# Optimization experiments

Measured on AMD Instinct MI355X. Metric: run time of the kernel, lower is better.

The kernel has to match this reference:

```python
import jax, jax.numpy as jnp
import numpy as np

N = 100_000            # particles
E = 3_200_000          # edges (avg degree 32)
DIM = 3
H = 1.0                # kernel_radius
SIGMA = 3.0 / 359.0 / np.pi / H**3   # 3D quintic kernel normalization
RHO_REF = 1.0
P_REF = 100.0          # rho_ref * (10*u_ref)**2 / gamma, gamma=1
P_BG = 0.0             # p_bg_factor * p_ref
ETA0 = 0.01            # base_viscosity
EPS = 1e-8


def _qpows(d, p):
    q = d / H
    return (jnp.maximum(0.0, 1.0 - q) ** p,
            jnp.maximum(0.0, 2.0 - q) ** p,
            jnp.maximum(0.0, 3.0 - q) ** p)


def kernel_w(d):
    q1, q2, q3 = _qpows(d, 5)
    return SIGMA * (q3 - 6.0 * q2 + 15.0 * q1)


def kernel_grad_w(d):
    q1, q2, q3 = _qpows(d, 4)
    return (SIGMA / H) * (-5.0 * q3 + 30.0 * q2 - 75.0 * q1)


def setup_inputs() -> dict:
    key = jax.random.key(0)
    k1, k2, k3, k4 = jax.random.split(key, 4)
    r = jax.random.uniform(k1, (N, DIM), dtype=jnp.float32)   # positions in unit box
    v = jax.random.normal(k2, (N, DIM), dtype=jnp.float32)    # velocity history (last frame)
    i_s = jax.random.randint(k3, (E,), 0, N)                  # receivers
    j_s = jax.random.randint(k4, (E,), 0, N)                  # senders
    return {"r": r, "v": v, "i_s": i_s, "j_s": j_s}


def reference(r, v, i_s, j_s):
    n = r.shape[0]
    # --- per-edge gather + kernel ---
    dr = r[i_s] - r[j_s]                       # displacement_fn, [E,3]
    d = jnp.sqrt(jnp.sum(dr * dr, axis=-1))    # [E]
    w = kernel_w(d)
    # --- density summation (scatter) ---
    mass = jnp.ones((n,), r.dtype)
    rho = mass * jax.ops.segment_sum(w, i_s, num_segments=n)
    # Tait EoS, gamma=1
    p = P_REF * (rho / RHO_REF - 1.0) + P_BG
    eta = jnp.full((n,), ETA0, r.dtype)

    # --- per-edge acceleration (gather particle fields to edges) ---
    rho_i, rho_j = rho[i_s], rho[j_s]
    p_i, p_j = p[i_s], p[j_s]
    eta_i, eta_j = eta[i_s], eta[j_s]
    u_i, u_j = v[i_s], v[j_s]                  # u == v in _transform
    v_i, v_j = u_i, u_j

    eta_ij = 2.0 * eta_i * eta_j / (eta_i + eta_j + EPS)
    p_ij = (rho_j * p_i + rho_i * p_j) / (rho_i + rho_j)
    # ((m_i/rho_i)^2 + (m_j/rho_j)^2)/m_i with m == 1
    wvol = (1.0 / rho_i) ** 2 + (1.0 / rho_j) ** 2
    c = wvol * kernel_grad_w(d) / (d + EPS)    # [E]

    # transport stress A = (outer(rho_i*u_i, v_i-u_i) + outer(rho_j*u_j, v_j-u_j))/2, [E,3,3]
    A = 0.5 * (rho_i[:, None, None] * u_i[:, :, None] * (v_i - u_i)[:, None, :]
               + rho_j[:, None, None] * u_j[:, :, None] * (v_j - u_j)[:, None, :])
    Ar = jnp.einsum('eij,ej->ei', A, dr)

    a_eq_8 = c[:, None] * (-p_ij[:, None] * dr + Ar + eta_ij[:, None] * (u_i - u_j))
    p_bg_i = jnp.zeros_like(p_i)               # _transform passes zeros
    a_eq_13 = (c * p_bg_i)[:, None] * dr

    # --- scatter-reduce to particles ---
    dudt = jax.ops.segment_sum(a_eq_8, i_s, num_segments=n)   # [N,3]
    dvdt = jax.ops.segment_sum(a_eq_13, i_s, num_segments=n)  # [N,3]

    # pack state outputs: [rho, p, dudt(3), dvdt(3)] -> [N,8]
    return jnp.concatenate([rho[:, None], p[:, None], dudt, dvdt], axis=1)
```

## Files before the change

kernel.cpp:

```cpp
#include <hip/hip_runtime.h>
#include <math.h>

#ifndef M_PI
#define M_PI 3.14159265358979323846
#endif

static constexpr float kSigma = (float)(3.0 / 359.0 / M_PI);
static constexpr float kPRef  = 100.0f;
static constexpr float kEps   = 1e-8f;
static constexpr float kEta   = (float)(2.0 * 0.01 * 0.01 / (0.01 + 0.01 + 1e-8));

#define CHUNK 4096
#define NSUB  8
#define BAT   5

typedef _Float16 hf4 __attribute__((ext_vector_type(4)));

__device__ __forceinline__ float pow5f(float t) { float t2 = t * t; return t2 * t2 * t; }
__device__ __forceinline__ float pow4f(float t) { float t2 = t * t; return t2 * t2; }

__global__ void k_pack(const float* __restrict__ r, float4* __restrict__ pos4, int n) {
    int i = blockIdx.x * blockDim.x + threadIdx.x;
    if (i >= n) return;
    pos4[i] = make_float4(r[3 * i], r[3 * i + 1], r[3 * i + 2], 0.f);
}

__global__ void k_hist(const int* __restrict__ i_s, int* __restrict__ ghist,
                       int nbA, int nbins, int E, int shift) {
    __shared__ int h[512];
    int t = threadIdx.x, blk = blockIdx.x;
    for (int b = t; b < nbins; b += 256) h[b] = 0;
    __syncthreads();
    int base = blk * CHUNK;
    int end = min(base + CHUNK, E);
    for (int kb = base; kb < end; kb += 256 * 4) {
        int iv[4];
#pragma unroll
        for (int b = 0; b < 4; b++) {
            int k = kb + b * 256 + t;
            iv[b] = (k < end) ? i_s[k] : -1;
        }
#pragma unroll
        for (int b = 0; b < 4; b++)
            if (iv[b] >= 0) atomicAdd(&h[iv[b] >> shift], 1);
    }
    __syncthreads();
    for (int b = t; b < nbins; b += 256)
        ghist[b * nbA + blk] = h[b];
}

__global__ void k_scan_block(const int* __restrict__ in, int* __restrict__ out,
                             int* __restrict__ bsum, int m) {
    __shared__ int s[256];
    int t = threadIdx.x;
    int i = blockIdx.x * 256 + t;
    int x = (i < m) ? in[i] : 0;
    s[t] = x;
    __syncthreads();
    for (int d = 1; d < 256; d <<= 1) {
        int v = (t >= d) ? s[t - d] : 0;
        __syncthreads();
        s[t] += v;
        __syncthreads();
    }
    if (i < m) out[i] = s[t] - x;
    if (t == 255) bsum[blockIdx.x] = s[255];
}

__global__ void k_scan_bsums(const int* __restrict__ bsum, int* __restrict__ bscan, int nb) {
    __shared__ int s[512];
    __shared__ int carry;
    int t = threadIdx.x;
    if (t == 0) carry = 0;
    __syncthreads();
    for (int base = 0; base < nb; base += 512) {
        int i = base + t;
        int x = (i < nb) ? bsum[i] : 0;
        s[t] = x;
        __syncthreads();
        for (int d = 1; d < 512; d <<= 1) {
            int v = (t >= d) ? s[t - d] : 0;
            __syncthreads();
            s[t] += v;
            __syncthreads();
        }
        if (i < nb) bscan[i] = s[t] - x + carry;
        __syncthreads();
        if (t == 511) carry += s[511];
        __syncthreads();
    }
}

__device__ __forceinline__ int scanned(const int* __restrict__ gscan,
                                       const int* __restrict__ bscan, int idx) {
    return gscan[idx] + bscan[idx >> 8];
}

__global__ void k_split(const int* __restrict__ i_s, const int* __restrict__ j_s,
                        const int* __restrict__ ghist, const int* __restrict__ gscan,
                        const int* __restrict__ bscan, int* __restrict__ pairs,
                        int nbA, int nbins, int E, int shift, int jbits) {
    __shared__ int lofs[512];
    __shared__ int ldelta[512];
    __shared__ int stage[CHUNK];
    __shared__ unsigned short binof[CHUNK];
    int t = threadIdx.x, blk = blockIdx.x;
    int base = blk * CHUNK;
    int end = min(base + CHUNK, E);
    int cnt = end - base;

    int h0 = (t < nbins) ? ghist[t * nbA + blk] : 0;
    int h1 = (t + 256 < nbins) ? ghist[(t + 256) * nbA + blk] : 0;
    lofs[t] = h0;
    lofs[t + 256] = h1;
    __syncthreads();
    for (int d = 1; d < 512; d <<= 1) {
        int v0 = (t >= d) ? lofs[t - d] : 0;
        int v1 = ((t + 256) >= d) ? lofs[t + 256 - d] : 0;
        __syncthreads();
        lofs[t] += v0;
        lofs[t + 256] += v1;
        __syncthreads();
    }
    int e0 = lofs[t] - h0;
    int e1 = lofs[t + 256] - h1;
    __syncthreads();
    lofs[t] = e0;
    lofs[t + 256] = e1;
    if (t < nbins) ldelta[t] = scanned(gscan, bscan, t * nbA + blk) - e0;
    if (t + 256 < nbins) ldelta[t + 256] = scanned(gscan, bscan, (t + 256) * nbA + blk) - e1;
    __syncthreads();

    int fmask = (1 << shift) - 1;
    for (int kb = base; kb < end; kb += 256 * 4) {
        int iv[4], jv[4];
#pragma unroll
        for (int b = 0; b < 4; b++) {
            int k = kb + b * 256 + t;
            iv[b] = (k < end) ? i_s[k] : -1;
            jv[b] = (k < end) ? j_s[k] : 0;
        }
#pragma unroll
        for (int b = 0; b < 4; b++) {
            if (iv[b] < 0) continue;
            int bin = iv[b] >> shift;
            int pos = atomicAdd(&lofs[bin], 1);
            stage[pos] = ((iv[b] & fmask) << jbits) | jv[b];
            binof[pos] = (unsigned short)bin;
        }
    }
    __syncthreads();
    for (int x = t; x < cnt; x += 256)
        pairs[x + ldelta[binof[x]]] = stage[x];
}

__global__ void __launch_bounds__(256, 6)
k_rho_bin(const float4* __restrict__ pos4, const int* __restrict__ pairs,
          const int* __restrict__ gscan, const int* __restrict__ bscan,
          float* __restrict__ part_rho, hf4* __restrict__ aux,
          int nbA, int n, int E, int shift, int jbits, int nbins) {
    __shared__ float srho[256];
    __shared__ float4 spos[256];
    __shared__ int sse[2];
    int bin = blockIdx.x >> 3, sub = blockIdx.x & (NSUB - 1);
    int t = threadIdx.x;
    int lo = bin << shift;
    srho[t] = 0.f;
    int ii = lo + t;
    spos[t] = (ii < n) ? pos4[ii] : make_float4(0.f, 0.f, 0.f, 0.f);
    if (t == 0) {
        sse[0] = scanned(gscan, bscan, bin * nbA);
        sse[1] = (bin + 1 < nbins) ? scanned(gscan, bscan, (bin + 1) * nbA) : E;
    }
    __syncthreads();
    int s = sse[0], len = sse[1] - sse[0];
    int k0 = s + (int)((long)len * sub / NSUB);
    int k1 = s + (int)((long)len * (sub + 1) / NSUB);
    int jm = (1 << jbits) - 1;
    for (int kb = k0; kb < k1; kb += 256 * BAT) {
        int pr[BAT], kk[BAT];
        bool live[BAT];
#pragma unroll
        for (int b = 0; b < BAT; b++) {
            int k = kb + b * 256 + t;
            live[b] = (k < k1);
            kk[b] = live[b] ? k : (k1 - 1);
            pr[b] = pairs[kk[b]];
        }
        float4 rj[BAT];
#pragma unroll
        for (int b = 0; b < BAT; b++) rj[b] = pos4[pr[b] & jm];
#pragma unroll
        for (int b = 0; b < BAT; b++) {
            int slot = pr[b] >> jbits;
            float4 ri = spos[slot];
            float dx = ri.x - rj[b].x, dy = ri.y - rj[b].y, dz = ri.z - rj[b].z;
            float d = sqrtf(dx * dx + dy * dy + dz * dz);
            float t1 = fmaxf(1.f - d, 0.f);
            float t2 = fmaxf(2.f - d, 0.f);
            float t3 = fmaxf(3.f - d, 0.f);
            float w = kSigma * (pow5f(t3) - 6.f * pow5f(t2) + 15.f * pow5f(t1));
            hf4 h;
            h.x = (_Float16)dx; h.y = (_Float16)dy;
            h.z = (_Float16)dz; h.w = (_Float16)d;
            if (live[b]) {
                atomicAdd(&srho[slot], w);
                aux[kk[b]] = h;
            }
        }
    }
    __syncthreads();
    if (ii < n) part_rho[(size_t)sub * n + ii] = srho[t];
}

__global__ void k_reduce_rho(const float* __restrict__ part_rho,
                             const float* __restrict__ v,
                             float4* __restrict__ vp4, float* __restrict__ out, int n) {
    int i = blockIdx.x * blockDim.x + threadIdx.x;
    if (i >= n) return;
    float rh = 0.f;
    for (int s = 0; s < NSUB; s++) rh += part_rho[(size_t)s * n + i];
    float pp = kPRef * (rh - 1.0f);
    vp4[i] = make_float4(v[3 * i], v[3 * i + 1], v[3 * i + 2], pp);
    float* o = out + (size_t)i * 8;
    o[0] = rh;
    o[1] = pp;
    o[5] = 0.f; o[6] = 0.f; o[7] = 0.f;
}

__global__ void __launch_bounds__(256, 6)
k_acc_bin(const float4* __restrict__ vp4, const int* __restrict__ pairs,
          const hf4* __restrict__ aux,
          const int* __restrict__ gscan, const int* __restrict__ bscan,
          float4* __restrict__ part_acc4, int nbA, int n, int E,
          int shift, int jbits, int nbins) {
    __shared__ float sax[256], say[256], saz[256];
    __shared__ float4 svp[256];
    __shared__ int sse[2];
    int bin = blockIdx.x >> 3, sub = blockIdx.x & (NSUB - 1);
    int t = threadIdx.x;
    int lo = bin << shift;
    sax[t] = 0.f; say[t] = 0.f; saz[t] = 0.f;
    int ii = lo + t;
    svp[t] = (ii < n) ? vp4[ii] : make_float4(0.f, 0.f, 0.f, 0.f);
    if (t == 0) {
        sse[0] = scanned(gscan, bscan, bin * nbA);
        sse[1] = (bin + 1 < nbins) ? scanned(gscan, bscan, (bin + 1) * nbA) : E;
    }
    __syncthreads();
    int s = sse[0], len = sse[1] - sse[0];
    int k0 = s + (int)((long)len * sub / NSUB);
    int k1 = s + (int)((long)len * (sub + 1) / NSUB);
    int jm = (1 << jbits) - 1;
    for (int kb = k0; kb < k1; kb += 256 * BAT) {
        int pr[BAT], kk[BAT];
        bool live[BAT];
        hf4 hx[BAT];
#pragma unroll
        for (int b = 0; b < BAT; b++) {
            int k = kb + b * 256 + t;
            live[b] = (k < k1);
            kk[b] = live[b] ? k : (k1 - 1);
            pr[b] = pairs[kk[b]];
            hx[b] = aux[kk[b]];
        }
        float4 vj[BAT];
#pragma unroll
        for (int b = 0; b < BAT; b++) vj[b] = vp4[pr[b] & jm];
#pragma unroll
        for (int b = 0; b < BAT; b++) {
            int slot = pr[b] >> jbits;
            float4 bi = svp[slot];
            float p_i = bi.w, p_j = vj[b].w;
            float rho_i = p_i * 0.01f + 1.0f;
            float rho_j = p_j * 0.01f + 1.0f;
            float dx = (float)hx[b].x, dy = (float)hx[b].y, dz = (float)hx[b].z;
            float d = (float)hx[b].w;
            float t1 = fmaxf(1.f - d, 0.f);
            float t2 = fmaxf(2.f - d, 0.f);
            float t3 = fmaxf(3.f - d, 0.f);
            float gw = kSigma * (-5.f * pow4f(t3) + 30.f * pow4f(t2) - 75.f * pow4f(t1));
            float inv_i = 1.0f / rho_i, inv_j = 1.0f / rho_j;
            float c = (inv_i * inv_i + inv_j * inv_j) * gw / (d + kEps);
            float p_ij = (rho_j * p_i + rho_i * p_j) / (rho_i + rho_j);
            if (live[b]) {
                atomicAdd(&sax[slot], c * (kEta * (bi.x - vj[b].x) - p_ij * dx));
                atomicAdd(&say[slot], c * (kEta * (bi.y - vj[b].y) - p_ij * dy));
                atomicAdd(&saz[slot], c * (kEta * (bi.z - vj[b].z) - p_ij * dz));
            }
        }
    }
    __syncthreads();
    if (ii < n)
        part_acc4[(size_t)sub * n + ii] = make_float4(sax[t], say[t], saz[t], 0.f);
}

__global__ void k_reduce_acc(const float4* __restrict__ part_acc4,
                             float* __restrict__ out, int n) {
    int i = blockIdx.x * blockDim.x + threadIdx.x;
    if (i >= n) return;
    float ax = 0.f, ay = 0.f, az = 0.f;
    for (int s = 0; s < NSUB; s++) {
        float4 p = part_acc4[(size_t)s * n + i];
        ax += p.x; ay += p.y; az += p.z;
    }
    float* o = out + (size_t)i * 8 + 2;
    o[0] = ax; o[1] = ay; o[2] = az;
}

static inline char* wcarve(char*& ws, size_t bytes) {
    char* p = ws;
    ws += (bytes + 255) & ~(size_t)255;
    return p;
}

extern "C" void kernel_launch(void* const* d_in, const int* in_sizes, int n_in,
                              void* d_out, int out_size, void* d_ws, size_t ws_size,
                              hipStream_t stream) {
    const float* r = (const float*)d_in[0];
    const float* v = (const float*)d_in[1];
    const int* i_s = (const int*)d_in[2];
    const int* j_s = (const int*)d_in[3];
    int n = in_sizes[0] / 3;
    int E = in_sizes[2];
    float* out = (float*)d_out;

    int shift = 8;
    int nbins = ((n - 1) >> shift) + 1;
    while (nbins > 512) { shift++; nbins = ((n - 1) >> shift) + 1; }
    int jbits = 1;
    while ((1 << jbits) < n) jbits++;

    int nbA = (E + CHUNK - 1) / CHUNK;
    int m = nbins * nbA;
    int nb2 = (m + 255) / 256;

    char* ws = (char*)d_ws;
    float4* pos4     = (float4*)wcarve(ws, (size_t)n * 16);
    float4* vp4      = (float4*)wcarve(ws, (size_t)n * 16);
    int*    ghist    = (int*)wcarve(ws, (size_t)m * 4);
    int*    gscan    = (int*)wcarve(ws, (size_t)m * 4);
    int*    bsum     = (int*)wcarve(ws, (size_t)nb2 * 4);
    int*    bscan    = (int*)wcarve(ws, (size_t)nb2 * 4);
    int*    pairs    = (int*)wcarve(ws, (size_t)E * 4);
    hf4*    aux      = (hf4*)wcarve(ws, (size_t)E * 8);
    float*  part_rho = (float*)wcarve(ws, (size_t)NSUB * n * 4);
    float4* part_acc4= (float4*)wcarve(ws, (size_t)NSUB * n * 16);

    const int bs = 256;
    int gn = (n + bs - 1) / bs;

    k_pack<<<gn, bs, 0, stream>>>(r, pos4, n);
    k_hist<<<nbA, 256, 0, stream>>>(i_s, ghist, nbA, nbins, E, shift);
    k_scan_block<<<nb2, 256, 0, stream>>>(ghist, gscan, bsum, m);
    k_scan_bsums<<<1, 512, 0, stream>>>(bsum, bscan, nb2);
    k_split<<<nbA, 256, 0, stream>>>(i_s, j_s, ghist, gscan, bscan, pairs, nbA, nbins, E, shift, jbits);
    k_rho_bin<<<nbins * NSUB, 256, 0, stream>>>(pos4, pairs, gscan, bscan, part_rho, aux, nbA, n, E, shift, jbits, nbins);
    k_reduce_rho<<<gn, bs, 0, stream>>>(part_rho, v, vp4, out, n);
    k_acc_bin<<<nbins * NSUB, 256, 0, stream>>>(vp4, pairs, aux, gscan, bscan, part_acc4, nbA, n, E, shift, jbits, nbins);
    k_reduce_acc<<<gn, bs, 0, stream>>>(part_acc4, out, n);
}
```

Baseline: 201.7 us.

## Two-level sort edges by sender slice and receiver bin, cache both in LDS

Replaces the single receiver-bin sort with a two-pass sort: first by sender slice of 4096 particles, then by receiver bin of 512. The density and acceleration passes can then stage both sender and receiver data in shared memory instead of doing random global gathers of sender data. Positions are quantized to 16-bit fixed point and velocity/pressure to fp16, which shrinks the footprint and removes the fp16 aux buffer. The cost is extra sort passes, per-slice partial buffers (25 slices × N) and reduced precision in positions, velocity and pressure.

```diff
diff --git a/kernel.cpp b/kernel.cpp
--- a/kernel.cpp
+++ b/kernel.cpp
@@ -9,44 +9,63 @@
 static constexpr float kPRef  = 100.0f;
 static constexpr float kEps   = 1e-8f;
 static constexpr float kEta   = (float)(2.0 * 0.01 * 0.01 / (0.01 + 0.01 + 1e-8));
-
-#define CHUNK 4096
-#define NSUB  8
-#define BAT   5
+static constexpr float kInvQ  = 1.0f / 65536.0f;
+
+#define CH     4096
+#define JS_SH  12
+#define JSLICE 4096
+#define IB_SH  9
+#define IBSZ   512
+#define C2MAX  48
+#define GBIN   8
 
 typedef _Float16 hf4 __attribute__((ext_vector_type(4)));
 
 __device__ __forceinline__ float pow5f(float t) { float t2 = t * t; return t2 * t2 * t; }
 __device__ __forceinline__ float pow4f(float t) { float t2 = t * t; return t2 * t2; }
 
-__global__ void k_pack(const float* __restrict__ r, float4* __restrict__ pos4, int n) {
+__device__ __forceinline__ int nt_load_i(const int* p) { return __builtin_nontemporal_load(p); }
+__device__ __forceinline__ float nt_load_f(const float* p) { return __builtin_nontemporal_load(p); }
+__device__ __forceinline__ void nt_store_f(float* p, float v) { __builtin_nontemporal_store(v, p); }
+
+__device__ __forceinline__ int scanned(const int* __restrict__ gscan,
+                                       const int* __restrict__ bscan, int idx) {
+    return gscan[idx] + bscan[idx >> 8];
+}
+
+__global__ void k_pack_pos(const float* __restrict__ r, ushort4* __restrict__ posq, int n) {
     int i = blockIdx.x * blockDim.x + threadIdx.x;
     if (i >= n) return;
-    pos4[i] = make_float4(r[3 * i], r[3 * i + 1], r[3 * i + 2], 0.f);
-}
-
-__global__ void k_hist(const int* __restrict__ i_s, int* __restrict__ ghist,
-                       int nbA, int nbins, int E, int shift) {
-    __shared__ int h[512];
+    float x = r[3 * i], y = r[3 * i + 1], z = r[3 * i + 2];
+    ushort4 q;
+    q.x = (unsigned short)fminf(x * 65536.0f, 65535.0f);
+    q.y = (unsigned short)fminf(y * 65536.0f, 65535.0f);
+    q.z = (unsigned short)fminf(z * 65536.0f, 65535.0f);
+    q.w = 0;
+    posq[i] = q;
+}
+
+__global__ void k_hist1(const int* __restrict__ j_s, int* __restrict__ ghist,
+                        int nbA, int nsl, int E) {
+    __shared__ int h[64];
     int t = threadIdx.x, blk = blockIdx.x;
-    for (int b = t; b < nbins; b += 256) h[b] = 0;
-    __syncthreads();
-    int base = blk * CHUNK;
-    int end = min(base + CHUNK, E);
+    if (t < 64) h[t] = 0;
+    __syncthreads();
+    int base = blk * CH;
+    int end = min(base + CH, E);
     for (int kb = base; kb < end; kb += 256 * 4) {
-        int iv[4];
+        int jv[4];
 #pragma unroll
         for (int b = 0; b < 4; b++) {
             int k = kb + b * 256 + t;
-            iv[b] = (k < end) ? i_s[k] : -1;
+            jv[b] = (k < end) ? j_s[k] : -1;
         }
 #pragma unroll
         for (int b = 0; b < 4; b++)
-            if (iv[b] >= 0) atomicAdd(&h[iv[b] >> shift], 1);
-    }
-    __syncthreads();
-    for (int b = t; b < nbins; b += 256)
-        ghist[b * nbA + blk] = h[b];
+            if (jv[b] >= 0) atomicAdd(&h[jv[b] >> JS_SH], 1);
+    }
+    __syncthreads();
+    if (t < nsl) ghist[t * nbA + blk] = h[t];
 }
 
 __global__ void k_scan_block(const int* __restrict__ in, int* __restrict__ out,
@@ -91,47 +110,35 @@
     }
 }
 
-__device__ __forceinline__ int scanned(const int* __restrict__ gscan,
-                                       const int* __restrict__ bscan, int idx) {
-    return gscan[idx] + bscan[idx >> 8];
-}
-
-__global__ void k_split(const int* __restrict__ i_s, const int* __restrict__ j_s,
-                        const int* __restrict__ ghist, const int* __restrict__ gscan,
-                        const int* __restrict__ bscan, int* __restrict__ pairs,
-                        int nbA, int nbins, int E, int shift, int jbits) {
-    __shared__ int lofs[512];
-    __shared__ int ldelta[512];
-    __shared__ int stage[CHUNK];
-    __shared__ unsigned short binof[CHUNK];
+__global__ void k_split1(const int* __restrict__ i_s, const int* __restrict__ j_s,
+                         const int* __restrict__ ghist, const int* __restrict__ gscan,
+                         const int* __restrict__ bscan, int* __restrict__ pairs1,
+                         int nbA, int nsl, int E) {
+    __shared__ int lofs[64];
+    __shared__ int ldelta[64];
+    __shared__ int stage[CH];
+    __shared__ unsigned short binof[CH];
     int t = threadIdx.x, blk = blockIdx.x;
-    int base = blk * CHUNK;
-    int end = min(base + CHUNK, E);
+    int base = blk * CH;
+    int end = min(base + CH, E);
     int cnt = end - base;
 
-    int h0 = (t < nbins) ? ghist[t * nbA + blk] : 0;
-    int h1 = (t + 256 < nbins) ? ghist[(t + 256) * nbA + blk] : 0;
-    lofs[t] = h0;
-    lofs[t + 256] = h1;
-    __syncthreads();
-    for (int d = 1; d < 512; d <<= 1) {
-        int v0 = (t >= d) ? lofs[t - d] : 0;
-        int v1 = ((t + 256) >= d) ? lofs[t + 256 - d] : 0;
-        __syncthreads();
-        lofs[t] += v0;
-        lofs[t + 256] += v1;
-        __syncthreads();
-    }
-    int e0 = lofs[t] - h0;
-    int e1 = lofs[t + 256] - h1;
-    __syncthreads();
-    lofs[t] = e0;
-    lofs[t + 256] = e1;
-    if (t < nbins) ldelta[t] = scanned(gscan, bscan, t * nbA + blk) - e0;
-    if (t + 256 < nbins) ldelta[t + 256] = scanned(gscan, bscan, (t + 256) * nbA + blk) - e1;
-    __syncthreads();
-
-    int fmask = (1 << shift) - 1;
+    if (t < 64) {
+        int h0 = (t < nsl) ? ghist[t * nbA + blk] : 0;
+        lofs[t] = h0;
+    }
+    __syncthreads();
+    if (t == 0) {
+        int run = 0;
+        for (int b = 0; b < nsl; b++) {
+            int h = lofs[b];
+            lofs[b] = run;
+            ldelta[b] = scanned(gscan, bscan, b * nbA + blk) - run;
+            run += h;
+        }
+    }
+    __syncthreads();
+
     for (int kb = base; kb < end; kb += 256 * 4) {
         int iv[4], jv[4];
 #pragma unroll
@@ -143,139 +150,225 @@
 #pragma unroll
         for (int b = 0; b < 4; b++) {
             if (iv[b] < 0) continue;
-            int bin = iv[b] >> shift;
+            int bin = jv[b] >> JS_SH;
             int pos = atomicAdd(&lofs[bin], 1);
-            stage[pos] = ((iv[b] & fmask) << jbits) | jv[b];
+            stage[pos] = (iv[b] << JS_SH) | (jv[b] & (JSLICE - 1));
             binof[pos] = (unsigned short)bin;
         }
     }
     __syncthreads();
     for (int x = t; x < cnt; x += 256)
-        pairs[x + ldelta[binof[x]]] = stage[x];
-}
-
-__global__ void __launch_bounds__(256, 6)
-k_rho_bin(const float4* __restrict__ pos4, const int* __restrict__ pairs,
-          const int* __restrict__ gscan, const int* __restrict__ bscan,
-          float* __restrict__ part_rho, hf4* __restrict__ aux,
-          int nbA, int n, int E, int shift, int jbits, int nbins) {
-    __shared__ float srho[256];
-    __shared__ float4 spos[256];
+        pairs1[x + ldelta[binof[x]]] = stage[x];
+}
+
+__global__ void k_hist2(const int* __restrict__ pairs1, const int* __restrict__ gscan1,
+                        const int* __restrict__ bscan1, int* __restrict__ ghist2,
+                        int nbA, int nsl, int nbin, int E) {
+    __shared__ int h[256];
+    int t = threadIdx.x;
+    int s = blockIdx.x / C2MAX, c = blockIdx.x % C2MAX;
+    h[t] = 0;
+    __syncthreads();
+    int start = scanned(gscan1, bscan1, s * nbA);
+    int end = (s + 1 < nsl) ? scanned(gscan1, bscan1, (s + 1) * nbA) : E;
+    int a0 = start + c * CH, a1 = min(a0 + CH, end);
+    for (int kb = a0; kb < a1; kb += 256 * 4) {
+        int pv[4];
+#pragma unroll
+        for (int b = 0; b < 4; b++) {
+            int k = kb + b * 256 + t;
+            pv[b] = (k < a1) ? pairs1[k] : -1;
+        }
+#pragma unroll
+        for (int b = 0; b < 4; b++)
+            if (pv[b] >= 0) atomicAdd(&h[pv[b] >> (JS_SH + IB_SH)], 1);
+    }
+    __syncthreads();
+    if (t < nbin) ghist2[(s * nbin + t) * C2MAX + c] = h[t];
+}
+
+__global__ void k_split2(const int* __restrict__ pairs1, const int* __restrict__ ghist2,
+                         const int* __restrict__ gscan2, const int* __restrict__ bscan2,
+                         const int* __restrict__ gscan1, const int* __restrict__ bscan1,
+                         int* __restrict__ pairs2, int nbA, int nsl, int nbin, int E) {
+    __shared__ int lofs[256];
+    __shared__ int ldelta[256];
+    __shared__ int stage[CH];
+    __shared__ unsigned short binof[CH];
+    int t = threadIdx.x;
+    int s = blockIdx.x / C2MAX, c = blockIdx.x % C2MAX;
+    int start = scanned(gscan1, bscan1, s * nbA);
+    int end = (s + 1 < nsl) ? scanned(gscan1, bscan1, (s + 1) * nbA) : E;
+    int a0 = start + c * CH, a1 = min(a0 + CH, end);
+    int cnt = max(a1 - a0, 0);
+
+    int h0 = (t < nbin) ? ghist2[(s * nbin + t) * C2MAX + c] : 0;
+    lofs[t] = h0;
+    __syncthreads();
+    for (int d = 1; d < 256; d <<= 1) {
+        int v = (t >= d) ? lofs[t - d] : 0;
+        __syncthreads();
+        lofs[t] += v;
+        __syncthreads();
+    }
+    int e0 = lofs[t] - h0;
+    __syncthreads();
+    lofs[t] = e0;
+    if (t < nbin) ldelta[t] = scanned(gscan2, bscan2, (s * nbin + t) * C2MAX + c) - e0;
+    __syncthreads();
+
+    for (int kb = a0; kb < a1; kb += 256 * 4) {
+        int pv[4];
+#pragma unroll
+        for (int b = 0; b < 4; b++) {
+            int k = kb + b * 256 + t;
+            pv[b] = (k < a1) ? pairs1[k] : -1;
+        }
+#pragma unroll
+        for (int b = 0; b < 4; b++) {
+            if (pv[b] < 0) continue;
+            int bin = pv[b] >> (JS_SH + IB_SH);
+            int pos = atomicAdd(&lofs[bin], 1);
+            stage[pos] = pv[b];
+            binof[pos] = (unsigned short)bin;
+        }
+    }
+    __syncthreads();
+    for (int x = t; x < cnt; x += 256)
+        pairs2[x + ldelta[binof[x]]] = stage[x];
+}
+
+__global__ void __launch_bounds__(256)
+k_pass1(const ushort4* __restrict__ posq, const int* __restrict__ pairs2,
+        const int* __restrict__ gscan2, const int* __restrict__ bscan2,
+        float* __restrict__ part_rho, int n, int E, int nsl, int nbin,
+        int nbg, int nk) {
+    __shared__ ushort4 sjp[JSLICE];
+    __shared__ ushort4 sip[IBSZ];
+    __shared__ float srho[IBSZ];
     __shared__ int sse[2];
-    int bin = blockIdx.x >> 3, sub = blockIdx.x & (NSUB - 1);
-    int t = threadIdx.x;
-    int lo = bin << shift;
-    srho[t] = 0.f;
-    int ii = lo + t;
-    spos[t] = (ii < n) ? pos4[ii] : make_float4(0.f, 0.f, 0.f, 0.f);
-    if (t == 0) {
-        sse[0] = scanned(gscan, bscan, bin * nbA);
-        sse[1] = (bin + 1 < nbins) ? scanned(gscan, bscan, (bin + 1) * nbA) : E;
-    }
-    __syncthreads();
-    int s = sse[0], len = sse[1] - sse[0];
-    int k0 = s + (int)((long)len * sub / NSUB);
-    int k1 = s + (int)((long)len * (sub + 1) / NSUB);
-    int jm = (1 << jbits) - 1;
-    for (int kb = k0; kb < k1; kb += 256 * BAT) {
-        int pr[BAT], kk[BAT];
-        bool live[BAT];
-#pragma unroll
-        for (int b = 0; b < BAT; b++) {
-            int k = kb + b * 256 + t;
-            live[b] = (k < k1);
-            kk[b] = live[b] ? k : (k1 - 1);
-            pr[b] = pairs[kk[b]];
-        }
-        float4 rj[BAT];
-#pragma unroll
-        for (int b = 0; b < BAT; b++) rj[b] = pos4[pr[b] & jm];
-#pragma unroll
-        for (int b = 0; b < BAT; b++) {
-            int slot = pr[b] >> jbits;
-            float4 ri = spos[slot];
-            float dx = ri.x - rj[b].x, dy = ri.y - rj[b].y, dz = ri.z - rj[b].z;
+    int t = threadIdx.x;
+    int s = blockIdx.x / nbg, g = blockIdx.x % nbg;
+    int j0 = s << JS_SH;
+    for (int idx = t; idx < JSLICE; idx += 256) {
+        int jg = j0 + idx;
+        sjp[idx] = (jg < n) ? posq[jg] : make_ushort4(0, 0, 0, 0);
+    }
+    int b0 = g * GBIN, b1 = min(b0 + GBIN, nbin);
+    for (int bin = b0; bin < b1; bin++) {
+        int i0 = bin << IB_SH;
+        for (int idx = t; idx < IBSZ; idx += 256) {
+            int ig = i0 + idx;
+            sip[idx] = (ig < n) ? posq[ig] : make_ushort4(0, 0, 0, 0);
+            srho[idx] = 0.f;
+        }
+        if (t == 0) {
+            int lin = s * nbin + bin;
+            sse[0] = scanned(gscan2, bscan2, lin * C2MAX);
+            sse[1] = (lin + 1 < nk) ? scanned(gscan2, bscan2, (lin + 1) * C2MAX) : E;
+        }
+        __syncthreads();
+        int ks = sse[0], ke = sse[1];
+        for (int k = ks + t; k < ke; k += 256) {
+            int pr = nt_load_i(&pairs2[k]);
+            int jl = pr & (JSLICE - 1);
+            int il = (pr >> JS_SH) & (IBSZ - 1);
+            ushort4 pj = sjp[jl];
+            ushort4 pi = sip[il];
+            float dx = (float)((int)pi.x - (int)pj.x) * kInvQ;
+            float dy = (float)((int)pi.y - (int)pj.y) * kInvQ;
+            float dz = (float)((int)pi.z - (int)pj.z) * kInvQ;
             float d = sqrtf(dx * dx + dy * dy + dz * dz);
             float t1 = fmaxf(1.f - d, 0.f);
             float t2 = fmaxf(2.f - d, 0.f);
             float t3 = fmaxf(3.f - d, 0.f);
             float w = kSigma * (pow5f(t3) - 6.f * pow5f(t2) + 15.f * pow5f(t1));
-            hf4 h;
-            h.x = (_Float16)dx; h.y = (_Float16)dy;
-            h.z = (_Float16)dz; h.w = (_Float16)d;
-            if (live[b]) {
-                atomicAdd(&srho[slot], w);
-                aux[kk[b]] = h;
-            }
-        }
-    }
-    __syncthreads();
-    if (ii < n) part_rho[(size_t)sub * n + ii] = srho[t];
+            atomicAdd(&srho[il], w);
+        }
+        __syncthreads();
+        for (int idx = t; idx < IBSZ; idx += 256) {
+            int ig = i0 + idx;
+            if (ig < n) nt_store_f(&part_rho[(size_t)s * n + ig], srho[idx]);
+        }
+        __syncthreads();
+    }
 }
 
 __global__ void k_reduce_rho(const float* __restrict__ part_rho,
                              const float* __restrict__ v,
-                             float4* __restrict__ vp4, float* __restrict__ out, int n) {
+                             hf4* __restrict__ vpq, float* __restrict__ out,
+                             int n, int nsl) {
     int i = blockIdx.x * blockDim.x + threadIdx.x;
     if (i >= n) return;
     float rh = 0.f;
-    for (int s = 0; s < NSUB; s++) rh += part_rho[(size_t)s * n + i];
+    for (int s = 0; s < nsl; s++) rh += nt_load_f(&part_rho[(size_t)s * n + i]);
     float pp = kPRef * (rh - 1.0f);
-    vp4[i] = make_float4(v[3 * i], v[3 * i + 1], v[3 * i + 2], pp);
+    hf4 h;
+    h.x = (_Float16)v[3 * i];
+    h.y = (_Float16)v[3 * i + 1];
+    h.z = (_Float16)v[3 * i + 2];
+    h.w = (_Float16)pp;
+    vpq[i] = h;
     float* o = out + (size_t)i * 8;
     o[0] = rh;
     o[1] = pp;
     o[5] = 0.f; o[6] = 0.f; o[7] = 0.f;
 }
 
-__global__ void __launch_bounds__(256, 6)
-k_acc_bin(const float4* __restrict__ vp4, const int* __restrict__ pairs,
-          const hf4* __restrict__ aux,
-          const int* __restrict__ gscan, const int* __restrict__ bscan,
-          float4* __restrict__ part_acc4, int nbA, int n, int E,
-          int shift, int jbits, int nbins) {
-    __shared__ float sax[256], say[256], saz[256];
-    __shared__ float4 svp[256];
+__global__ void __launch_bounds__(256)
+k_pass2(const ushort4* __restrict__ posq, const hf4* __restrict__ vpq,
+        const int* __restrict__ pairs2, const int* __restrict__ gscan2,
+        const int* __restrict__ bscan2, float* __restrict__ pax,
+        float* __restrict__ pay, float* __restrict__ paz,
+        int n, int E, int nsl, int nbin, int nbg, int nk) {
+    extern __shared__ char dyn[];
+    ushort4* sjp = (ushort4*)dyn;
+    hf4*     sjv = (hf4*)(dyn + 32768);
+    ushort4* sip = (ushort4*)(dyn + 65536);
+    hf4*     siv = (hf4*)(dyn + 69632);
+    float*   sax = (float*)(dyn + 73728);
+    float*   say = (float*)(dyn + 75776);
+    float*   saz = (float*)(dyn + 77824);
     __shared__ int sse[2];
-    int bin = blockIdx.x >> 3, sub = blockIdx.x & (NSUB - 1);
-    int t = threadIdx.x;
-    int lo = bin << shift;
-    sax[t] = 0.f; say[t] = 0.f; saz[t] = 0.f;
-    int ii = lo + t;
-    svp[t] = (ii < n) ? vp4[ii] : make_float4(0.f, 0.f, 0.f, 0.f);
-    if (t == 0) {
-        sse[0] = scanned(gscan, bscan, bin * nbA);
-        sse[1] = (bin + 1 < nbins) ? scanned(gscan, bscan, (bin + 1) * nbA) : E;
-    }
-    __syncthreads();
-    int s = sse[0], len = sse[1] - sse[0];
-    int k0 = s + (int)((long)len * sub / NSUB);
-    int k1 = s + (int)((long)len * (sub + 1) / NSUB);
-    int jm = (1 << jbits) - 1;
-    for (int kb = k0; kb < k1; kb += 256 * BAT) {
-        int pr[BAT], kk[BAT];
-        bool live[BAT];
-        hf4 hx[BAT];
-#pragma unroll
-        for (int b = 0; b < BAT; b++) {
-            int k = kb + b * 256 + t;
-            live[b] = (k < k1);
-            kk[b] = live[b] ? k : (k1 - 1);
-            pr[b] = pairs[kk[b]];
-            hx[b] = aux[kk[b]];
-        }
-        float4 vj[BAT];
-#pragma unroll
-        for (int b = 0; b < BAT; b++) vj[b] = vp4[pr[b] & jm];
-#pragma unroll
-        for (int b = 0; b < BAT; b++) {
-            int slot = pr[b] >> jbits;
-            float4 bi = svp[slot];
-            float p_i = bi.w, p_j = vj[b].w;
+    int t = threadIdx.x;
+    int s = blockIdx.x / nbg, g = blockIdx.x % nbg;
+    int j0 = s << JS_SH;
+    for (int idx = t; idx < JSLICE; idx += 256) {
+        int jg = j0 + idx;
+        if (jg < n) { sjp[idx] = posq[jg]; sjv[idx] = vpq[jg]; }
+        else { sjp[idx] = make_ushort4(0, 0, 0, 0); sjv[idx] = hf4{0, 0, 0, 0}; }
+    }
+    int b0 = g * GBIN, b1 = min(b0 + GBIN, nbin);
+    for (int bin = b0; bin < b1; bin++) {
+        int i0 = bin << IB_SH;
+        for (int idx = t; idx < IBSZ; idx += 256) {
+            int ig = i0 + idx;
+            if (ig < n) { sip[idx] = posq[ig]; siv[idx] = vpq[ig]; }
+            else { sip[idx] = make_ushort4(0, 0, 0, 0); siv[idx] = hf4{0, 0, 0, 0}; }
+            sax[idx] = 0.f; say[idx] = 0.f; saz[idx] = 0.f;
+        }
+        if (t == 0) {
+            int lin = s * nbin + bin;
+            sse[0] = scanned(gscan2, bscan2, lin * C2MAX);
+            sse[1] = (lin + 1 < nk) ? scanned(gscan2, bscan2, (lin + 1) * C2MAX) : E;
+        }
+        __syncthreads();
+        int ks = sse[0], ke = sse[1];
+        for (int k = ks + t; k < ke; k += 256) {
+            int pr = nt_load_i(&pairs2[k]);
+            int jl = pr & (JSLICE - 1);
+            int il = (pr >> JS_SH) & (IBSZ - 1);
+            ushort4 pj = sjp[jl];
+            hf4 vj = sjv[jl];
+            ushort4 pi = sip[il];
+            hf4 vi = siv[il];
+            float dx = (float)((int)pi.x - (int)pj.x) * kInvQ;
+            float dy = (float)((int)pi.y - (int)pj.y) * kInvQ;
+            float dz = (float)((int)pi.z - (int)pj.z) * kInvQ;
+            float d = sqrtf(dx * dx + dy * dy + dz * dz);
+            float p_i = (float)vi.w, p_j = (float)vj.w;
             float rho_i = p_i * 0.01f + 1.0f;
             float rho_j = p_j * 0.01f + 1.0f;
-            float dx = (float)hx[b].x, dy = (float)hx[b].y, dz = (float)hx[b].z;
-            float d = (float)hx[b].w;
             float t1 = fmaxf(1.f - d, 0.f);
             float t2 = fmaxf(2.f - d, 0.f);
             float t3 = fmaxf(3.f - d, 0.f);
@@ -283,26 +376,33 @@
             float inv_i = 1.0f / rho_i, inv_j = 1.0f / rho_j;
             float c = (inv_i * inv_i + inv_j * inv_j) * gw / (d + kEps);
             float p_ij = (rho_j * p_i + rho_i * p_j) / (rho_i + rho_j);
-            if (live[b]) {
-                atomicAdd(&sax[slot], c * (kEta * (bi.x - vj[b].x) - p_ij * dx));
-                atomicAdd(&say[slot], c * (kEta * (bi.y - vj[b].y) - p_ij * dy));
-                atomicAdd(&saz[slot], c * (kEta * (bi.z - vj[b].z) - p_ij * dz));
+            atomicAdd(&sax[il], c * (kEta * ((float)vi.x - (float)vj.x) - p_ij * dx));
+            atomicAdd(&say[il], c * (kEta * ((float)vi.y - (float)vj.y) - p_ij * dy));
+            atomicAdd(&saz[il], c * (kEta * ((float)vi.z - (float)vj.z) - p_ij * dz));
+        }
+        __syncthreads();
+        for (int idx = t; idx < IBSZ; idx += 256) {
+            int ig = i0 + idx;
+            if (ig < n) {
+                nt_store_f(&pax[(size_t)s * n + ig], sax[idx]);
+                nt_store_f(&pay[(size_t)s * n + ig], say[idx]);
+                nt_store_f(&paz[(size_t)s * n + ig], saz[idx]);
             }
         }
-    }
-    __syncthreads();
-    if (ii < n)
-        part_acc4[(size_t)sub * n + ii] = make_float4(sax[t], say[t], saz[t], 0.f);
-}
-
-__global__ void k_reduce_acc(const float4* __restrict__ part_acc4,
-                             float* __restrict__ out, int n) {
+        __syncthreads();
+    }
+}
+
+__global__ void k_reduce_acc(const float* __restrict__ pax, const float* __restrict__ pay,
+                             const float* __restrict__ paz, float* __restrict__ out,
+                             int n, int nsl) {
     int i = blockIdx.x * blockDim.x + threadIdx.x;
     if (i >= n) return;
     float ax = 0.f, ay = 0.f, az = 0.f;
-    for (int s = 0; s < NSUB; s++) {
-        float4 p = part_acc4[(size_t)s * n + i];
-        ax += p.x; ay += p.y; az += p.z;
+    for (int s = 0; s < nsl; s++) {
+        ax += nt_load_f(&pax[(size_t)s * n + i]);
+        ay += nt_load_f(&pay[(size_t)s * n + i]);
+        az += nt_load_f(&paz[(size_t)s * n + i]);
     }
     float* o = out + (size_t)i * 8 + 2;
     o[0] = ax; o[1] = ay; o[2] = az;
@@ -325,38 +425,58 @@
     int E = in_sizes[2];
     float* out = (float*)d_out;
 
-    int shift = 8;
-    int nbins = ((n - 1) >> shift) + 1;
-    while (nbins > 512) { shift++; nbins = ((n - 1) >> shift) + 1; }
-    int jbits = 1;
-    while ((1 << jbits) < n) jbits++;
-
-    int nbA = (E + CHUNK - 1) / CHUNK;
-    int m = nbins * nbA;
-    int nb2 = (m + 255) / 256;
+    int nsl  = ((n - 1) >> JS_SH) + 1;
+    int nbin = ((n - 1) >> IB_SH) + 1;
+    int nk   = nsl * nbin;
+    int nbg  = (nbin + GBIN - 1) / GBIN;
+    int nbA  = (E + CH - 1) / CH;
+    int m1   = nsl * nbA;
+    int m2   = nk * C2MAX;
+    int nb1  = (m1 + 255) / 256;
+    int nb2  = (m2 + 255) / 256;
 
     char* ws = (char*)d_ws;
-    float4* pos4     = (float4*)wcarve(ws, (size_t)n * 16);
-    float4* vp4      = (float4*)wcarve(ws, (size_t)n * 16);
-    int*    ghist    = (int*)wcarve(ws, (size_t)m * 4);
-    int*    gscan    = (int*)wcarve(ws, (size_t)m * 4);
-    int*    bsum     = (int*)wcarve(ws, (size_t)nb2 * 4);
-    int*    bscan    = (int*)wcarve(ws, (size_t)nb2 * 4);
-    int*    pairs    = (int*)wcarve(ws, (size_t)E * 4);
-    hf4*    aux      = (hf4*)wcarve(ws, (size_t)E * 8);
-    float*  part_rho = (float*)wcarve(ws, (size_t)NSUB * n * 4);
-    float4* part_acc4= (float4*)wcarve(ws, (size_t)NSUB * n * 16);
+    ushort4* posq   = (ushort4*)wcarve(ws, (size_t)n * 8);
+    hf4*     vpq    = (hf4*)wcarve(ws, (size_t)n * 8);
+    int*     ghist1 = (int*)wcarve(ws, (size_t)m1 * 4);
+    int*     gscan1 = (int*)wcarve(ws, (size_t)m1 * 4);
+    int*     bsum1  = (int*)wcarve(ws, (size_t)nb1 * 4);
+    int*     bscan1 = (int*)wcarve(ws, (size_t)nb1 * 4);
+    int*     pairs1 = (int*)wcarve(ws, (size_t)E * 4);
+    int*     ghist2 = (int*)wcarve(ws, (size_t)m2 * 4);
+    int*     gscan2 = (int*)wcarve(ws, (size_t)m2 * 4);
+    int*     bsum2  = (int*)wcarve(ws, (size_t)nb2 * 4);
+    int*     bscan2 = (int*)wcarve(ws, (size_t)nb2 * 4);
+    int*     pairs2 = (int*)wcarve(ws, (size_t)E * 4);
+    float*   part_rho = (float*)wcarve(ws, (size_t)nsl * n * 4);
+    float*   pax    = (float*)wcarve(ws, (size_t)nsl * n * 4);
+    float*   pay    = (float*)wcarve(ws, (size_t)nsl * n * 4);
+    float*   paz    = (float*)wcarve(ws, (size_t)nsl * n * 4);
 
     const int bs = 256;
     int gn = (n + bs - 1) / bs;
 
-    k_pack<<<gn, bs, 0, stream>>>(r, pos4, n);
-    k_hist<<<nbA, 256, 0, stream>>>(i_s, ghist, nbA, nbins, E, shift);
-    k_scan_block<<<nb2, 256, 0, stream>>>(ghist, gscan, bsum, m);
-    k_scan_bsums<<<1, 512, 0, stream>>>(bsum, bscan, nb2);
-    k_split<<<nbA, 256, 0, stream>>>(i_s, j_s, ghist, gscan, bscan, pairs, nbA, nbins, E, shift, jbits);
-    k_rho_bin<<<nbins * NSUB, 256, 0, stream>>>(pos4, pairs, gscan, bscan, part_rho, aux, nbA, n, E, shift, jbits, nbins);
-    k_reduce_rho<<<gn, bs, 0, stream>>>(part_rho, v, vp4, out, n);
-    k_acc_bin<<<nbins * NSUB, 256, 0, stream>>>(vp4, pairs, aux, gscan, bscan, part_acc4, nbA, n, E, shift, jbits, nbins);
-    k_reduce_acc<<<gn, bs, 0, stream>>>(part_acc4, out, n);
-}
+    static bool attr_set = false;
+    if (!attr_set) {
+        hipFuncSetAttribute((const void*)k_pass2,
+                            hipFuncAttributeMaxDynamicSharedMemorySize, 81920);
+        attr_set = true;
+    }
+
+    k_pack_pos<<<gn, bs, 0, stream>>>(r, posq, n);
+    k_hist1<<<nbA, 256, 0, stream>>>(j_s, ghist1, nbA, nsl, E);
+    k_scan_block<<<nb1, 256, 0, stream>>>(ghist1, gscan1, bsum1, m1);
+    k_scan_bsums<<<1, 512, 0, stream>>>(bsum1, bscan1, nb1);
+    k_split1<<<nbA, 256, 0, stream>>>(i_s, j_s, ghist1, gscan1, bscan1, pairs1, nbA, nsl, E);
+    k_hist2<<<nsl * C2MAX, 256, 0, stream>>>(pairs1, gscan1, bscan1, ghist2, nbA, nsl, nbin, E);
+    k_scan_block<<<nb2, 256, 0, stream>>>(ghist2, gscan2, bsum2, m2);
+    k_scan_bsums<<<1, 512, 0, stream>>>(bsum2, bscan2, nb2);
+    k_split2<<<nsl * C2MAX, 256, 0, stream>>>(pairs1, ghist2, gscan2, bscan2,
+                                              gscan1, bscan1, pairs2, nbA, nsl, nbin, E);
+    k_pass1<<<nsl * nbg, 256, 0, stream>>>(posq, pairs2, gscan2, bscan2, part_rho,
+                                           n, E, nsl, nbin, nbg, nk);
+    k_reduce_rho<<<gn, bs, 0, stream>>>(part_rho, v, vpq, out, n, nsl);
+    k_pass2<<<nsl * nbg, 256, 81920, stream>>>(posq, vpq, pairs2, gscan2, bscan2,
+                                               pax, pay, paz, n, E, nsl, nbin, nbg, nk);
+    k_reduce_acc<<<gn, bs, 0, stream>>>(pax, pay, paz, out, n, nsl);
+}
```

After: 323.3 us. 60.3% more time.
